# Optimization experiments

Measured on AMD Instinct MI355X. Metric: run time of the kernel, lower is better.

## Reference

```python
import math
import jax, jax.numpy as jnp
import numpy as np

N_EMBD = 768
N_HEAD = 12
BLOCK_SIZE = 1024
B, T, N_ENC = 8, 1024, 257
EPS = 1e-5


def _ln(x, g, b):
    m = jnp.mean(x, axis=-1, keepdims=True)
    v = jnp.var(x, axis=-1, keepdims=True)
    return (x - m) * jax.lax.rsqrt(v + EPS) * g + b


def _heads(t, n_head):
    B_, N_, C_ = t.shape
    return t.reshape(B_, N_, n_head, C_ // n_head).transpose(0, 2, 1, 3)  # [B,H,N,D]


def setup_inputs() -> dict:
    key = jax.random.key(0)
    ks = jax.random.split(key, 16)
    s = 0.02
    d, h4, dq = N_EMBD, 4 * N_EMBD, N_EMBD // 4
    inp = {
        'x': jax.random.normal(ks[0], (B, T, d), jnp.float32),
        'x_enc': jax.random.normal(ks[1], (B, N_ENC, d), jnp.float32),
        'ln1_g': jnp.ones((d,), jnp.float32), 'ln1_b': jnp.zeros((d,), jnp.float32),
        'ln2_g': jnp.ones((d,), jnp.float32), 'ln2_b': jnp.zeros((d,), jnp.float32),
        'ln3_g': jnp.ones((d,), jnp.float32), 'ln3_b': jnp.zeros((d,), jnp.float32),
        'attn_w': jax.random.normal(ks[2], (d, 3 * d), jnp.float32) * s,
        'attn_bias': jnp.zeros((3 * d,), jnp.float32),
        'attn_proj_w': jax.random.normal(ks[3], (d, d), jnp.float32) * s,
        'attn_proj_b': jnp.zeros((d,), jnp.float32),
        'img_w': jax.random.normal(ks[4], (d, 2 * d), jnp.float32) * s,
        'img_b': jnp.zeros((2 * d,), jnp.float32),
        'cap_w': jax.random.normal(ks[5], (d, d), jnp.float32) * s,
        'cap_b': jnp.zeros((d,), jnp.float32),
        'cross_proj_w': jax.random.normal(ks[6], (d, d), jnp.float32) * s,
        'cross_proj_b': jnp.zeros((d,), jnp.float32),
        'ad1_w': jax.random.normal(ks[7], (d, dq), jnp.float32) * s,
        'ad1_b': jnp.zeros((dq,), jnp.float32),
        'ad2_w': jax.random.normal(ks[8], (dq, d), jnp.float32) * s,
        'ad2_b': jnp.zeros((d,), jnp.float32),
        'fc_w': jax.random.normal(ks[9], (d, h4), jnp.float32) * s,
        'fc_b': jnp.zeros((h4,), jnp.float32),
        'mproj_w': jax.random.normal(ks[10], (h4, d), jnp.float32) * s,
        'mproj_b': jnp.zeros((d,), jnp.float32),
    }
    return inp


def _block(x, x_enc, ln1_g, ln1_b, ln2_g, ln2_b, ln3_g, ln3_b,
           attn_w, attn_bias, attn_proj_w, attn_proj_b,
           img_w, img_b, cap_w, cap_b, cross_proj_w, cross_proj_b,
           ad1_w, ad1_b, ad2_w, ad2_b, fc_w, fc_b, mproj_w, mproj_b):
    d, nh = N_EMBD, N_HEAD
    hd = d // nh
    scale = 1.0 / math.sqrt(hd)

    def adapter(h):
        return jax.nn.relu(h @ ad1_w + ad1_b) @ ad2_w + ad2_b

    # --- causal self-attention ---
    h = _ln(x, ln1_g, ln1_b)
    qkv = h @ attn_w + attn_bias
    q, k, v = jnp.split(qkv, 3, axis=2)
    q, k, v = _heads(q, nh), _heads(k, nh), _heads(v, nh)  # [B,H,T,hd]
    att = jnp.einsum('bhqd,bhkd->bhqk', q, k) * scale
    Tq = x.shape[1]
    causal = jnp.tril(jnp.ones((Tq, Tq), bool))
    att = jnp.where(causal, att, -jnp.inf)
    att = jax.nn.softmax(att, axis=-1)
    sa = jnp.einsum('bhqk,bhkd->bhqd', att, v).transpose(0, 2, 1, 3).reshape(x.shape)
    sa = sa @ attn_proj_w + attn_proj_b
    x = x + adapter(sa)

    # --- cross-attention (queries from x, keys/values from x_enc) ---
    hq = _ln(x, ln1_g, ln1_b)
    he = _ln(x_enc, ln3_g, ln3_b)
    kv = he @ img_w + img_b
    k2, v2 = jnp.split(kv, 2, axis=2)
    q2 = hq @ cap_w + cap_b
    q2, k2, v2 = _heads(q2, nh), _heads(k2, nh), _heads(v2, nh)
    catt = jax.nn.softmax(jnp.einsum('bhqd,bhkd->bhqk', q2, k2) * scale, axis=-1)
    ca = jnp.einsum('bhqk,bhkd->bhqd', catt, v2).transpose(0, 2, 1, 3).reshape(x.shape)
    ca = ca @ cross_proj_w + cross_proj_b
    x = x + adapter(ca)

    # --- MLP ---
    hm = _ln(x, ln2_g, ln2_b)
    m = jax.nn.gelu(hm @ fc_w + fc_b, approximate=True) @ mproj_w + mproj_b
    x = x + adapter(m)
    return x, x_enc


def reference(x, x_enc, ln1_g, ln1_b, ln2_g, ln2_b, ln3_g, ln3_b,
              attn_w, attn_bias, attn_proj_w, attn_proj_b,
              img_w, img_b, cap_w, cap_b, cross_proj_w, cross_proj_b,
              ad1_w, ad1_b, ad2_w, ad2_b, fc_w, fc_b, mproj_w, mproj_b):
    return _block(x, x_enc, ln1_g, ln1_b, ln2_g, ln2_b, ln3_g, ln3_b,
                  attn_w, attn_bias, attn_proj_w, attn_proj_b,
                  img_w, img_b, cap_w, cap_b, cross_proj_w, cross_proj_b,
                  ad1_w, ad1_b, ad2_w, ad2_b, fc_w, fc_b, mproj_w, mproj_b)
```

## Files before the change

kernel.cpp:

```cpp
#include <hip/hip_runtime.h>

typedef unsigned short u16;
typedef short bf16x8 __attribute__((ext_vector_type(8)));
typedef float f32x4 __attribute__((ext_vector_type(4)));
typedef unsigned short u16x4 __attribute__((ext_vector_type(4)));

__device__ __forceinline__ u16 f2bf(float f) {
  union { float f; unsigned u; } v; v.f = f;
  unsigned u = v.u;
  unsigned r = (u + 0x7FFFu + ((u >> 16) & 1u)) >> 16;
  return (u16)r;
}
__device__ __forceinline__ float bf2f(u16 h) {
  union { unsigned u; float f; } v; v.u = ((unsigned)h) << 16;
  return v.f;
}
__device__ __forceinline__ unsigned cvt_pk_bf16(float lo, float hi) {
  unsigned d;
  asm("v_cvt_pk_bf16_f32 %0, %1, %2" : "=v"(d) : "v"(lo), "v"(hi));
  return d;
}
__device__ __forceinline__ float gelu_f(float x) {
  const float c1 = -2.302585093f;
  const float c2 = -0.1029620967f;
  float t = __builtin_fmaf(x * x, c2, c1) * x;
  float e = exp2f(t);
  return x * __builtin_amdgcn_rcpf(e + 1.0f);
}

#define GLD_LDS16(gp, lp)                                             \
  __builtin_amdgcn_global_load_lds(                                   \
      (const __attribute__((address_space(1))) void*)(gp),            \
      (__attribute__((address_space(3))) void*)(lp), 16, 0, 0)

template<int OFF>
__device__ __forceinline__ u16x4 tr16(unsigned a) {
  u16x4 d;
  asm volatile("ds_read_b64_tr_b16 %0, %1 offset:%2" : "=&v"(d) : "v"(a), "n"(OFF));
  return d;
}
__device__ __forceinline__ bf16x8 pack8(u16x4 a, u16x4 b) {
  union { u16x4 p[2]; bf16x8 v; } u;
  u.p[0] = a; u.p[1] = b;
  return u.v;
}
__device__ __forceinline__ u16x4 pack4(unsigned w0, unsigned w1) {
  union { unsigned w[2]; u16x4 v; } u;
  u.w[0] = w0; u.w[1] = w1;
  return u.v;
}

struct TrBatch {
  const float* W[9];
  u16* Bt[9];
  int K[9], N[9], Kpad[9], Npad[9];
  int tstart[10];
};
__global__ __launch_bounds__(256)
void transpose_all(TrBatch tb) {
  __shared__ float tile[64][65];
  const int tid = blockIdx.x;
  int mi = 0;
  while (mi < 8 && tid >= tb.tstart[mi + 1]) ++mi;
  const int lt = tid - tb.tstart[mi];
  const int tx = tb.Npad[mi] >> 6;
  const int n0 = (lt % tx) * 64;
  const int k0 = (lt / tx) * 64;
  const float* W = tb.W[mi];
  u16* Bt = tb.Bt[mi];
  const int K = tb.K[mi], N = tb.N[mi], Kpad = tb.Kpad[mi];
  const int t = threadIdx.x;
  const int c = t & 63;
  const int rb = t >> 6;
#pragma unroll
  for (int i = 0; i < 16; ++i) {
    int r = i * 4 + rb;
    float v = 0.f;
    if (k0 + r < K && n0 + c < N) v = W[(size_t)(k0 + r) * N + n0 + c];
    tile[r][c] = v;
  }
  __syncthreads();
#pragma unroll
  for (int i = 0; i < 16; ++i) {
    int r = i * 4 + rb;
    Bt[(size_t)(n0 + r) * Kpad + k0 + c] = f2bf(tile[c][r]);
  }
}

__global__ __launch_bounds__(64)
void ln_kernel(const float* __restrict__ X, const float* __restrict__ G,
               const float* __restrict__ Bv, u16* __restrict__ O, int Mreal) {
  const int row = blockIdx.x;
  const int l = threadIdx.x;
  u16* op = O + (size_t)row * 768;
  if (row >= Mreal) {
    u16x4 z = {0, 0, 0, 0};
#pragma unroll
    for (int i = 0; i < 3; ++i) *(u16x4*)(op + (i * 64 + l) * 4) = z;
    return;
  }
  const float* xp = X + (size_t)row * 768;
  float v[12];
  float s = 0.f, s2 = 0.f;
#pragma unroll
  for (int i = 0; i < 3; ++i) {
    float4 t4 = *(const float4*)(xp + (i * 64 + l) * 4);
    v[i * 4 + 0] = t4.x; v[i * 4 + 1] = t4.y; v[i * 4 + 2] = t4.z; v[i * 4 + 3] = t4.w;
    s += t4.x + t4.y + t4.z + t4.w;
    s2 += t4.x * t4.x + t4.y * t4.y + t4.z * t4.z + t4.w * t4.w;
  }
#pragma unroll
  for (int off = 32; off > 0; off >>= 1) {
    s += __shfl_xor(s, off);
    s2 += __shfl_xor(s2, off);
  }
  const float mean = s * (1.0f / 768.0f);
  const float var = s2 * (1.0f / 768.0f) - mean * mean;
  const float rstd = rsqrtf(var + 1e-5f);
#pragma unroll
  for (int i = 0; i < 3; ++i) {
    int base = (i * 64 + l) * 4;
    float4 g4 = *(const float4*)(G + base);
    float4 b4 = *(const float4*)(Bv + base);
    u16x4 o4;
    o4[0] = f2bf((v[i * 4 + 0] - mean) * rstd * g4.x + b4.x);
    o4[1] = f2bf((v[i * 4 + 1] - mean) * rstd * g4.y + b4.y);
    o4[2] = f2bf((v[i * 4 + 2] - mean) * rstd * g4.z + b4.z);
    o4[3] = f2bf((v[i * 4 + 3] - mean) * rstd * g4.w + b4.w);
    *(u16x4*)(op + base) = o4;
  }
}

template<bool DOLN, bool RESID>
__global__ __launch_bounds__(64)
void resid_ln(const float* __restrict__ S, float* __restrict__ D,
              const u16* __restrict__ P,
              const float* __restrict__ G, const float* __restrict__ Bv,
              u16* __restrict__ O) {
  const int row = blockIdx.x;
  const int l = threadIdx.x;
  const float* sp = S + (size_t)row * 768;
  float* dp = D + (size_t)row * 768;
  float v[12];
  float s = 0.f, s2 = 0.f;
#pragma unroll
  for (int i = 0; i < 3; ++i) {
    const int base = (i * 64 + l) * 4;
    float4 t4 = *(const float4*)(sp + base);
    if (RESID) {
      u16x4 p4 = *(const u16x4*)(P + (size_t)row * 768 + base);
      t4.x += bf2f(p4[0]); t4.y += bf2f(p4[1]);
      t4.z += bf2f(p4[2]); t4.w += bf2f(p4[3]);
    }
    v[i * 4 + 0] = t4.x; v[i * 4 + 1] = t4.y; v[i * 4 + 2] = t4.z; v[i * 4 + 3] = t4.w;
    s += t4.x + t4.y + t4.z + t4.w;
    s2 += t4.x * t4.x + t4.y * t4.y + t4.z * t4.z + t4.w * t4.w;
    *(float4*)(dp + base) = t4;
  }
  if (DOLN) {
#pragma unroll
    for (int off = 32; off > 0; off >>= 1) {
      s += __shfl_xor(s, off);
      s2 += __shfl_xor(s2, off);
    }
    const float mean = s * (1.0f / 768.0f);
    const float var = s2 * (1.0f / 768.0f) - mean * mean;
    const float rstd = rsqrtf(var + 1e-5f);
    u16* op = O + (size_t)row * 768;
#pragma unroll
    for (int i = 0; i < 3; ++i) {
      int base = (i * 64 + l) * 4;
      float4 g4 = *(const float4*)(G + base);
      float4 b4 = *(const float4*)(Bv + base);
      u16x4 o4;
      o4[0] = f2bf((v[i * 4 + 0] - mean) * rstd * g4.x + b4.x);
      o4[1] = f2bf((v[i * 4 + 1] - mean) * rstd * g4.y + b4.y);
      o4[2] = f2bf((v[i * 4 + 2] - mean) * rstd * g4.z + b4.z);
      o4[3] = f2bf((v[i * 4 + 3] - mean) * rstd * g4.w + b4.w);
      *(u16x4*)(op + base) = o4;
    }
  }
}

template<int MODE>
__global__ void gemm_bt(const u16* __restrict__ A, const u16* __restrict__ Bt,
                        void* __restrict__ C, const float* __restrict__ bias,
                        int K, int ldc, int nbias) {
  __shared__ u16 As[2 * 128 * 32];
  __shared__ u16 Bs[2 * 128 * 32];
  const int t = threadIdx.x;
  const int lane = t & 63;
  const int wid = t >> 6;
  const int wm = (wid >> 1) * 64;
  const int wn = (wid & 1) * 64;
  const int tm = blockIdx.x * 128;
  const int tn = blockIdx.y * 128;

  f32x4 zero = {0.f, 0.f, 0.f, 0.f};
  f32x4 acc[4][4];
#pragma unroll
  for (int i = 0; i < 4; ++i)
#pragma unroll
    for (int j = 0; j < 4; ++j) acc[i][j] = zero;

  const int rowA = lane & 15;
  const int kb = (((lane >> 4) ^ ((rowA >> 1) & 3)) << 3);
  const int kTiles = K >> 6;
  for (int kt = 0; kt < kTiles; ++kt) {
    const int kk = kt << 6;
#pragma unroll
    for (int i = 0; i < 4; ++i) {
      const int c = i * 256 + t;
      const int r = (c >> 2) & 127;
      const int cc = ((c >> 9) << 5) + ((((c & 3) ^ ((r >> 1) & 3))) << 3);
      GLD_LDS16(A + (size_t)(tm + r) * K + kk + cc, As + c * 8);
      GLD_LDS16(Bt + (size_t)(tn + r) * K + kk + cc, Bs + c * 8);
    }
    __syncthreads();
#pragma unroll
    for (int ks = 0; ks < 2; ++ks) {
      bf16x8 af[4], bfr[4];
      const int base = ks * 4096;
#pragma unroll
      for (int i = 0; i < 4; ++i) {
        af[i] = *(const bf16x8*)(As + base + (wm + i * 16 + rowA) * 32 + kb);
        bfr[i] = *(const bf16x8*)(Bs + base + (wn + i * 16 + rowA) * 32 + kb);
      }
#pragma unroll
      for (int mi = 0; mi < 4; ++mi)
#pragma unroll
        for (int ni = 0; ni < 4; ++ni)
          acc[mi][ni] = __builtin_amdgcn_mfma_f32_16x16x32_bf16(af[mi], bfr[ni], acc[mi][ni], 0, 0, 0);
    }
    __syncthreads();
  }
  const int col0 = lane & 15;
  const int row0 = (lane >> 4) << 2;
#pragma unroll
  for (int mi = 0; mi < 4; ++mi) {
#pragma unroll
    for (int ni = 0; ni < 4; ++ni) {
      int col = tn + wn + ni * 16 + col0;
      float bb = (col < nbias) ? bias[col] : 0.f;
      float vv[4];
#pragma unroll
      for (int r = 0; r < 4; ++r) {
        float v = acc[mi][ni][r] + bb;
        if (MODE == 1) v = fmaxf(v, 0.f);
        else if (MODE == 2) v = gelu_f(v);
        vv[r] = v;
      }
      unsigned w0 = cvt_pk_bf16(vv[0], vv[1]);
      unsigned w1 = cvt_pk_bf16(vv[2], vv[3]);
      size_t row = (size_t)(tm + wm + mi * 16 + row0);
      u16* cp = (u16*)C + row * ldc + col;
      cp[0] = (u16)w0;
      cp[(size_t)ldc] = (u16)(w0 >> 16);
      cp[(size_t)ldc * 2] = (u16)w1;
      cp[(size_t)ldc * 3] = (u16)(w1 >> 16);
    }
  }
}

template<int MODE>
__global__ __launch_bounds__(256)
void gemm_bt_k128(const u16* __restrict__ A, const u16* __restrict__ Bt,
                  void* __restrict__ C, const float* __restrict__ bias,
                  int K, int ldc, int nbias) {
  __shared__ u16 As[4 * 128 * 32];
  __shared__ u16 Bs[4 * 128 * 32];
  const int t = threadIdx.x;
  const int lane = t & 63;
  const int wid = t >> 6;
  const int wm = (wid >> 1) * 64;
  const int wn = (wid & 1) * 64;
  const int tm = blockIdx.x * 128;
  const int tn = blockIdx.y * 128;

  f32x4 zero = {0.f, 0.f, 0.f, 0.f};
  f32x4 acc[4][4];
#pragma unroll
  for (int i = 0; i < 4; ++i)
#pragma unroll
    for (int j = 0; j < 4; ++j) acc[i][j] = zero;

  const int rowA = lane & 15;
  const int kb = (((lane >> 4) ^ ((rowA >> 1) & 3)) << 3);
  const int kTiles = K >> 7;
  for (int kt = 0; kt < kTiles; ++kt) {
    const int kk = kt << 7;
#pragma unroll
    for (int i = 0; i < 8; ++i) {
      const int c = i * 256 + t;
      const int r = (c >> 2) & 127;
      const int cc = ((c >> 9) << 5) + ((((c & 3) ^ ((r >> 1) & 3))) << 3);
      GLD_LDS16(A + (size_t)(tm + r) * K + kk + cc, As + c * 8);
      GLD_LDS16(Bt + (size_t)(tn + r) * K + kk + cc, Bs + c * 8);
    }
    __syncthreads();
#pragma unroll
    for (int ks = 0; ks < 4; ++ks) {
      bf16x8 af[4], bfr[4];
      const int base = ks * 4096;
#pragma unroll
      for (int i = 0; i < 4; ++i) {
        af[i] = *(const bf16x8*)(As + base + (wm + i * 16 + rowA) * 32 + kb);
        bfr[i] = *(const bf16x8*)(Bs + base + (wn + i * 16 + rowA) * 32 + kb);
      }
#pragma unroll
      for (int mi = 0; mi < 4; ++mi)
#pragma unroll
        for (int ni = 0; ni < 4; ++ni)
          acc[mi][ni] = __builtin_amdgcn_mfma_f32_16x16x32_bf16(af[mi], bfr[ni], acc[mi][ni], 0, 0, 0);
    }
    __syncthreads();
  }
  const int col0 = lane & 15;
  const int row0 = (lane >> 4) << 2;
#pragma unroll
  for (int mi = 0; mi < 4; ++mi) {
#pragma unroll
    for (int ni = 0; ni < 4; ++ni) {
      int col = tn + wn + ni * 16 + col0;
      float bb = (col < nbias) ? bias[col] : 0.f;
      float vv[4];
#pragma unroll
      for (int r = 0; r < 4; ++r) {
        float v = acc[mi][ni][r] + bb;
        if (MODE == 1) v = fmaxf(v, 0.f);
        vv[r] = v;
      }
      unsigned w0 = cvt_pk_bf16(vv[0], vv[1]);
      unsigned w1 = cvt_pk_bf16(vv[2], vv[3]);
      size_t row = (size_t)(tm + wm + mi * 16 + row0);
      u16* cp = (u16*)C + row * ldc + col;
      cp[0] = (u16)w0;
      cp[(size_t)ldc] = (u16)(w0 >> 16);
      cp[(size_t)ldc * 2] = (u16)w1;
      cp[(size_t)ldc * 3] = (u16)(w1 >> 16);
    }
  }
}

struct GemmJob {
  const u16* A; const u16* Bt; u16* C; const float* bias;
  int K, ldc, nbias, mblocks;
};
__global__ __launch_bounds__(256)
void gemm_bt_dual(GemmJob j0, GemmJob j1, int split) {
  __shared__ u16 As[2 * 128 * 32];
  __shared__ u16 Bs[2 * 128 * 32];
  const int bid = blockIdx.x;
  const GemmJob& J = (bid < split) ? j0 : j1;
  const int lb = (bid < split) ? bid : bid - split;
  const int tm = (lb % J.mblocks) * 128;
  const int tn = (lb / J.mblocks) * 128;
  const u16* A = J.A;
  const u16* Bt = J.Bt;
  const int K = J.K;

  const int t = threadIdx.x;
  const int lane = t & 63;
  const int wid = t >> 6;
  const int wm = (wid >> 1) * 64;
  const int wn = (wid & 1) * 64;

  f32x4 zero = {0.f, 0.f, 0.f, 0.f};
  f32x4 acc[4][4];
#pragma unroll
  for (int i = 0; i < 4; ++i)
#pragma unroll
    for (int j = 0; j < 4; ++j) acc[i][j] = zero;

  const int rowA = lane & 15;
  const int kb = (((lane >> 4) ^ ((rowA >> 1) & 3)) << 3);
  const int kTiles = K >> 6;
  for (int kt = 0; kt < kTiles; ++kt) {
    const int kk = kt << 6;
#pragma unroll
    for (int i = 0; i < 4; ++i) {
      const int c = i * 256 + t;
      const int r = (c >> 2) & 127;
      const int cc = ((c >> 9) << 5) + ((((c & 3) ^ ((r >> 1) & 3))) << 3);
      GLD_LDS16(A + (size_t)(tm + r) * K + kk + cc, As + c * 8);
      GLD_LDS16(Bt + (size_t)(tn + r) * K + kk + cc, Bs + c * 8);
    }
    __syncthreads();
#pragma unroll
    for (int ks = 0; ks < 2; ++ks) {
      bf16x8 af[4], bfr[4];
      const int base = ks * 4096;
#pragma unroll
      for (int i = 0; i < 4; ++i) {
        af[i] = *(const bf16x8*)(As + base + (wm + i * 16 + rowA) * 32 + kb);
        bfr[i] = *(const bf16x8*)(Bs + base + (wn + i * 16 + rowA) * 32 + kb);
      }
#pragma unroll
      for (int mi = 0; mi < 4; ++mi)
#pragma unroll
        for (int ni = 0; ni < 4; ++ni)
          acc[mi][ni] = __builtin_amdgcn_mfma_f32_16x16x32_bf16(af[mi], bfr[ni], acc[mi][ni], 0, 0, 0);
    }
    __syncthreads();
  }
  const int col0 = lane & 15;
  const int row0 = (lane >> 4) << 2;
#pragma unroll
  for (int mi = 0; mi < 4; ++mi) {
#pragma unroll
    for (int ni = 0; ni < 4; ++ni) {
      int col = tn + wn + ni * 16 + col0;
      float bb = (col < J.nbias) ? J.bias[col] : 0.f;
      unsigned w0 = cvt_pk_bf16(acc[mi][ni][0] + bb, acc[mi][ni][1] + bb);
      unsigned w1 = cvt_pk_bf16(acc[mi][ni][2] + bb, acc[mi][ni][3] + bb);
      size_t row = (size_t)(tm + wm + mi * 16 + row0);
      u16* cp = J.C + row * J.ldc + col;
      cp[0] = (u16)w0;
      cp[(size_t)J.ldc] = (u16)(w0 >> 16);
      cp[(size_t)J.ldc * 2] = (u16)w1;
      cp[(size_t)J.ldc * 3] = (u16)(w1 >> 16);
    }
  }
}

template<bool CAUSAL>
__global__ __launch_bounds__(256)
void attn_mfma(const u16* __restrict__ Q, const u16* __restrict__ Kp,
               const u16* __restrict__ Vp,
               u16* __restrict__ O0, u16* __restrict__ O1, float2* __restrict__ ML,
               int seqkv, int qrs, int krs,
               long long qBatch, long long kBatch,
               int qoff, int koff, int voff) {
  __shared__ __align__(16) u16 Ks[64 * 64];
  __shared__ __align__(16) u16 Vs[4096];
  __shared__ __align__(16) u16 Ps[4][1024];
  const int t = threadIdx.x;
  const int lane = t & 63;
  const int wid = t >> 6;
  const int b = blockIdx.x / 12, h = blockIdx.x % 12;
  const int yq = CAUSAL ? ((int)gridDim.y - 1 - (int)blockIdx.y) : (int)blockIdx.y;
  const int q0 = yq * 64;
  const int colid = lane & 15;
  const int rgrp = lane >> 4;
  const int z = CAUSAL ? blockIdx.z : 0;

  int kt_begin = 0, kt_end;
  if (CAUSAL) {
    const int ntr = yq + 1;
    const int half = (ntr + 1) >> 1;
    kt_begin = z ? half : 0;
    kt_end = z ? ntr : half;
  } else {
    kt_end = (seqkv + 63) >> 6;
  }
  u16* Op = (CAUSAL && z) ? O1 : O0;

  if (CAUSAL && kt_begin >= kt_end) {
    if (colid == 0) {
#pragma unroll
      for (int r = 0; r < 4; ++r) {
        int qrow = q0 + wid * 16 + rgrp * 4 + r;
        ML[((size_t)z * 8192 + b * 1024 + qrow) * 12 + h] = make_float2(-1e30f, 0.f);
      }
    }
    return;
  }

  const u16* qp = Q + (size_t)b * qBatch + qoff + (size_t)(q0 + wid * 16 + colid) * qrs + h * 64;
  bf16x8 qa[2];
#pragma unroll
  for (int s = 0; s < 2; ++s) qa[s] = *(const bf16x8*)(qp + s * 32 + (rgrp << 3));

  f32x4 oacc[4];
#pragma unroll
  for (int i = 0; i < 4; ++i) oacc[i] = (f32x4){0.f, 0.f, 0.f, 0.f};
  float m[4] = {-1e30f, -1e30f, -1e30f, -1e30f};
  float l[4] = {0.f, 0.f, 0.f, 0.f};

  const u16* kbase = Kp + (size_t)b * kBatch + koff + h * 64;
  const u16* vbase = Vp + (size_t)b * kBatch + voff + h * 64;

  const int srr = t >> 3, sdc = t & 7;
  int kwo[2], vwo[2];
#pragma unroll
  for (int i = 0; i < 2; ++i) {
    const int r = srr + 32 * i;
    kwo[i] = r * 64 + ((sdc ^ (r & 7)) << 3);
    vwo[i] = ((sdc >> 1) << 10) + (i << 9) + (((srr >> 2) & 1) << 8)
           + (((srr >> 3) & 3) << 6) + ((srr & 3) << 4) + (((2 * sdc) & 3) << 2);
  }
  const unsigned vs_base = (unsigned)(size_t)&Vs[0] + 8u * (unsigned)lane;
  const unsigned ps_base = (unsigned)(size_t)&Ps[wid][0] + 8u * (unsigned)lane;

  bf16x8 kz[2], vz[2];
  auto LOADT = [&](int kt) {
    const int k0 = kt * 64;
#pragma unroll
    for (int i = 0; i < 2; ++i) {
      const int tk = k0 + srr + 32 * i;
      const int dc = sdc << 3;
      kz[i] = (bf16x8){0, 0, 0, 0, 0, 0, 0, 0};
      vz[i] = (bf16x8){0, 0, 0, 0, 0, 0, 0, 0};
      if (tk < seqkv) {
        kz[i] = *(const bf16x8*)(kbase + (size_t)tk * krs + dc);
        vz[i] = *(const bf16x8*)(vbase + (size_t)tk * krs + dc);
      }
    }
  };
  LOADT(kt_begin);

  constexpr float SC2 = 0.18033688011112042f;

  for (int kt = kt_begin; kt < kt_end; ++kt) {
    const int k0 = kt * 64;
#pragma unroll
    for (int i = 0; i < 2; ++i) {
      *(bf16x8*)&Ks[kwo[i]] = kz[i];
      *(bf16x8*)&Vs[vwo[i]] = vz[i];
    }
    __syncthreads();
    if (kt + 1 < kt_end) LOADT(kt + 1);

    f32x4 sacc[4];
#pragma unroll
    for (int c = 0; c < 4; ++c) sacc[c] = (f32x4){0.f, 0.f, 0.f, 0.f};
#pragma unroll
    for (int c = 0; c < 4; ++c)
#pragma unroll
      for (int s = 0; s < 2; ++s) {
        bf16x8 kf = *(const bf16x8*)&Ks[(c * 16 + colid) * 64 +
                                        ((((s << 2) + rgrp) ^ (colid & 7)) << 3)];
        sacc[c] = __builtin_amdgcn_mfma_f32_16x16x32_bf16(qa[s], kf, sacc[c], 0, 0, 0);
      }

    const bool domask = CAUSAL ? (kt == yq) : (kt == kt_end - 1);
    if (domask) {
#pragma unroll
      for (int c = 0; c < 4; ++c) {
        int kv = k0 + c * 16 + colid;
#pragma unroll
        for (int r = 0; r < 4; ++r) {
          int q = q0 + wid * 16 + rgrp * 4 + r;
          if ((CAUSAL && kv > q) || (!CAUSAL && kv >= seqkv)) sacc[c][r] = -1e30f;
        }
      }
    }

    float pms[4];
#pragma unroll
    for (int r = 0; r < 4; ++r) {
      float v = fmaxf(fmaxf(sacc[0][r], sacc[1][r]), fmaxf(sacc[2][r], sacc[3][r]));
#pragma unroll
      for (int off = 1; off < 16; off <<= 1) v = fmaxf(v, __shfl_xor(v, off));
      pms[r] = v * SC2;
    }
    bool ok = (pms[0] <= m[0] + 8.f) && (pms[1] <= m[1] + 8.f) &&
              (pms[2] <= m[2] + 8.f) && (pms[3] <= m[3] + 8.f);
    if (!__all(ok)) {
#pragma unroll
      for (int r = 0; r < 4; ++r) {
        float newm = fmaxf(m[r], pms[r]);
        float corr = exp2f(m[r] - newm);
        m[r] = newm;
        l[r] *= corr;
#pragma unroll
        for (int dc2 = 0; dc2 < 4; ++dc2) oacc[dc2][r] *= corr;
      }
    }

    float pv[4][4];
    float psum[4] = {0.f, 0.f, 0.f, 0.f};
#pragma unroll
    for (int c = 0; c < 4; ++c)
#pragma unroll
      for (int r = 0; r < 4; ++r) {
        float p = exp2f(__builtin_fmaf(sacc[c][r], SC2, -m[r]));
        pv[c][r] = p;
        psum[r] += p;
      }
#pragma unroll
    for (int r = 0; r < 4; ++r) {
#pragma unroll
      for (int off = 1; off < 16; off <<= 1) psum[r] += __shfl_xor(psum[r], off);
      l[r] += psum[r];
    }

#pragma unroll
    for (int c = 0; c < 4; ++c) {
      unsigned w0 = cvt_pk_bf16(pv[c][0], pv[c][1]);
      unsigned w1 = cvt_pk_bf16(pv[c][2], pv[c][3]);
      const int pa = ((c >> 1) << 9) + (((colid >> 2) & 1) << 8)
                   + (((2 * c + (colid >> 3)) & 3) << 6) + ((colid & 3) << 4) + (rgrp << 2);
      *(u16x4*)&Ps[wid][pa] = pack4(w0, w1);
    }
    __builtin_amdgcn_sched_barrier(0);

    u16x4 p00 = tr16<0>(ps_base);
    u16x4 p01 = tr16<512>(ps_base);
    u16x4 p10 = tr16<1024>(ps_base);
    u16x4 p11 = tr16<1536>(ps_base);
    asm volatile("s_waitcnt lgkmcnt(0)" ::: "memory");
    __builtin_amdgcn_sched_barrier(0);
    bf16x8 pf0 = pack8(p00, p01);
    bf16x8 pf1 = pack8(p10, p11);

#pragma unroll
    for (int dc2 = 0; dc2 < 4; ++dc2) {
      const unsigned va = vs_base + (unsigned)(dc2 * 2048);
      u16x4 v00 = tr16<0>(va);
      u16x4 v01 = tr16<512>(va);
      u16x4 v10 = tr16<1024>(va);
      u16x4 v11 = tr16<1536>(va);
      asm volatile("s_waitcnt lgkmcnt(0)" ::: "memory");
      __builtin_amdgcn_sched_barrier(0);
      bf16x8 vf0 = pack8(v00, v01);
      bf16x8 vf1 = pack8(v10, v11);
      oacc[dc2] = __builtin_amdgcn_mfma_f32_16x16x32_bf16(pf0, vf0, oacc[dc2], 0, 0, 0);
      oacc[dc2] = __builtin_amdgcn_mfma_f32_16x16x32_bf16(pf1, vf1, oacc[dc2], 0, 0, 0);
    }
    __syncthreads();
  }

#pragma unroll
  for (int r = 0; r < 4; ++r) {
    int qrow = q0 + wid * 16 + rgrp * 4 + r;
    u16* op = Op + ((size_t)b * 1024 + qrow) * 768 + h * 64;
    if (CAUSAL) {
      unsigned w0 = cvt_pk_bf16(oacc[0][r], oacc[1][r]);
      unsigned w1 = cvt_pk_bf16(oacc[2][r], oacc[3][r]);
      op[colid] = (u16)w0;
      op[16 + colid] = (u16)(w0 >> 16);
      op[32 + colid] = (u16)w1;
      op[48 + colid] = (u16)(w1 >> 16);
      if (colid == 0)
        ML[((size_t)z * 8192 + b * 1024 + qrow) * 12 + h] = make_float2(m[r], l[r]);
    } else {
      float inv = 1.f / l[r];
      unsigned w0 = cvt_pk_bf16(oacc[0][r] * inv, oacc[1][r] * inv);
      unsigned w1 = cvt_pk_bf16(oacc[2][r] * inv, oacc[3][r] * inv);
      op[colid] = (u16)w0;
      op[16 + colid] = (u16)(w0 >> 16);
      op[32 + colid] = (u16)w1;
      op[48 + colid] = (u16)(w1 >> 16);
    }
  }
}

__global__ __launch_bounds__(64)
void attn_combine(const u16* __restrict__ P0, const u16* __restrict__ P1,
                  const float2* __restrict__ ML, u16* __restrict__ O) {
  const int row = blockIdx.x;
  const int l = threadIdx.x;
#pragma unroll
  for (int i = 0; i < 3; ++i) {
    const int base = (i * 64 + l) * 4;
    const int h = base >> 6;
    float2 ml0 = ML[(size_t)row * 12 + h];
    float2 ml1 = ML[(size_t)8192 * 12 + row * 12 + h];
    float mm = fmaxf(ml0.x, ml1.x);
    float w0 = exp2f(ml0.x - mm);
    float w1 = exp2f(ml1.x - mm);
    float inv = 1.f / (ml0.y * w0 + ml1.y * w1);
    u16x4 a = *(const u16x4*)(P0 + (size_t)row * 768 + base);
    u16x4 c = *(const u16x4*)(P1 + (size_t)row * 768 + base);
    u16x4 o4;
#pragma unroll
    for (int j = 0; j < 4; ++j)
      o4[j] = f2bf((bf2f(a[j]) * w0 + bf2f(c[j]) * w1) * inv);
    *(u16x4*)(O + (size_t)row * 768 + base) = o4;
  }
}

extern "C" void kernel_launch(void* const* d_in, const int* in_sizes, int n_in,
                              void* d_out, int out_size, void* d_ws, size_t ws_size,
                              hipStream_t stream) {
  const float* x        = (const float*)d_in[0];
  const float* x_enc    = (const float*)d_in[1];
  const float* ln1_g    = (const float*)d_in[2];
  const float* ln1_b    = (const float*)d_in[3];
  const float* ln2_g    = (const float*)d_in[4];
  const float* ln2_b    = (const float*)d_in[5];
  const float* ln3_g    = (const float*)d_in[6];
  const float* ln3_b    = (const float*)d_in[7];
  const float* attn_w   = (const float*)d_in[8];
  const float* attn_bias= (const float*)d_in[9];
  const float* proj_w   = (const float*)d_in[10];
  const float* proj_b   = (const float*)d_in[11];
  const float* img_w    = (const float*)d_in[12];
  const float* img_b    = (const float*)d_in[13];
  const float* cap_w    = (const float*)d_in[14];
  const float* cap_b    = (const float*)d_in[15];
  const float* cross_w  = (const float*)d_in[16];
  const float* cross_b  = (const float*)d_in[17];
  const float* ad1_w    = (const float*)d_in[18];
  const float* ad1_b    = (const float*)d_in[19];
  const float* ad2_w    = (const float*)d_in[20];
  const float* ad2_b    = (const float*)d_in[21];
  const float* fc_w     = (const float*)d_in[22];
  const float* fc_b     = (const float*)d_in[23];
  const float* mproj_w  = (const float*)d_in[24];
  const float* mproj_b  = (const float*)d_in[25];

  const int Mx = 8192;
  const int Me = 2056;
  const int MeP = 2176;

  float* out_x  = (float*)d_out;
  float* out_xe = out_x + (size_t)Mx * 768;

  char* ws = (char*)d_ws;
  size_t off = 0;
  auto alloc = [&](size_t elems) {
    u16* p = (u16*)(ws + off);
    off = (off + elems * 2 + 255) & ~(size_t)255;
    return p;
  };
  u16* wt_attn  = alloc((size_t)2304 * 768);
  u16* wt_proj  = alloc((size_t)768 * 768);
  u16* wt_img   = alloc((size_t)1536 * 768);
  u16* wt_cap   = alloc((size_t)768 * 768);
  u16* wt_cross = alloc((size_t)768 * 768);
  u16* wt_ad1   = alloc((size_t)256 * 768);
  u16* wt_ad2   = alloc((size_t)768 * 256);
  u16* wt_fc    = alloc((size_t)3072 * 768);
  u16* wt_mproj = alloc((size_t)768 * 3072);
  u16* hbuf     = alloc((size_t)Mx * 768);
  u16* big      = alloc((size_t)Mx * 3072);
  u16* p0       = alloc((size_t)Mx * 768);
  u16* p1       = alloc((size_t)Mx * 768);
  u16* hid      = alloc((size_t)Mx * 256);
  float2* mlbuf = (float2*)alloc((size_t)2 * 8192 * 12 * 4);
  u16* q2  = big;
  u16* kvb = big + (size_t)Mx * 768;

  hipMemcpyAsync(out_xe, x_enc, (size_t)Me * 768 * 4, hipMemcpyDeviceToDevice, stream);

  TrBatch tb;
  int nt = 0;
  tb.tstart[0] = 0;
  auto addT = [&](const float* W, u16* Bt, int K, int N, int Kp, int Np) {
    tb.W[nt] = W; tb.Bt[nt] = Bt; tb.K[nt] = K; tb.N[nt] = N;
    tb.Kpad[nt] = Kp; tb.Npad[nt] = Np;
    tb.tstart[nt + 1] = tb.tstart[nt] + (Np / 64) * (Kp / 64);
    ++nt;
  };
  addT(attn_w, wt_attn, 768, 2304, 768, 2304);
  addT(proj_w, wt_proj, 768, 768, 768, 768);
  addT(img_w, wt_img, 768, 1536, 768, 1536);
  addT(cap_w, wt_cap, 768, 768, 768, 768);
  addT(cross_w, wt_cross, 768, 768, 768, 768);
  addT(ad1_w, wt_ad1, 768, 192, 768, 256);
  addT(ad2_w, wt_ad2, 192, 768, 256, 768);
  addT(fc_w, wt_fc, 768, 3072, 768, 3072);
  addT(mproj_w, wt_mproj, 3072, 768, 3072, 768);
  transpose_all<<<tb.tstart[9], 256, 0, stream>>>(tb);

  auto GEMM = [&](const u16* A, const u16* Bt, void* C, const float* bias,
                  int M, int N, int K, int ldc, int nbias, int mode) {
    dim3 g(M / 128, N / 128);
    if (mode == 0)      gemm_bt<0><<<g, 256, 0, stream>>>(A, Bt, C, bias, K, ldc, nbias);
    else if (mode == 1) gemm_bt<1><<<g, 256, 0, stream>>>(A, Bt, C, bias, K, ldc, nbias);
    else                gemm_bt<2><<<g, 256, 0, stream>>>(A, Bt, C, bias, K, ldc, nbias);
  };
  auto GEMM_K128 = [&](const u16* A, const u16* Bt, void* C, const float* bias,
                       int M, int N, int K, int ldc, int nbias, int mode) {
    dim3 g(M / 128, N / 128);
    if (mode == 0) gemm_bt_k128<0><<<g, 256, 0, stream>>>(A, Bt, C, bias, K, ldc, nbias);
    else           gemm_bt_k128<1><<<g, 256, 0, stream>>>(A, Bt, C, bias, K, ldc, nbias);
  };
  auto ADAPTER = [&](const u16* in, u16* padw) {
    GEMM_K128(in, wt_ad1, hid, ad1_b, Mx, 256, 768, 256, 192, 1);
    GEMM_K128(hid, wt_ad2, padw, ad2_b, Mx, 768, 256, 768, 768, 0);
  };

  resid_ln<true, false><<<Mx, 64, 0, stream>>>(x, out_x, nullptr, ln1_g, ln1_b, hbuf);

  GEMM(hbuf, wt_attn, big, attn_bias, Mx, 2304, 768, 2304, 2304, 0);
  attn_mfma<true><<<dim3(96, 16, 2), 256, 0, stream>>>(
      big, big, big, hbuf, p1, mlbuf, 1024, 2304, 2304,
      (long long)1024 * 2304, (long long)1024 * 2304, 0, 768, 1536);
  attn_combine<<<Mx, 64, 0, stream>>>(hbuf, p1, mlbuf, p0);
  GEMM_K128(p0, wt_proj, p1, proj_b, Mx, 768, 768, 768, 768, 0);
  ADAPTER(p1, p0);
  resid_ln<true, true><<<Mx, 64, 0, stream>>>(out_x, out_x, p0, ln1_g, ln1_b, hbuf);

  ln_kernel<<<MeP, 64, 0, stream>>>(x_enc, ln3_g, ln3_b, p0, Me);
  {
    GemmJob jkv = { p0,   wt_img, kvb, img_b, 768, 1536, 1536, MeP / 128 };
    GemmJob jq2 = { hbuf, wt_cap, q2,  cap_b, 768, 768,  768,  Mx / 128 };
    const int split = (MeP / 128) * (1536 / 128);
    const int total = split + (Mx / 128) * (768 / 128);
    gemm_bt_dual<<<total, 256, 0, stream>>>(jkv, jq2, split);
  }
  attn_mfma<false><<<dim3(96, 16), 256, 0, stream>>>(
      q2, kvb, kvb, p1, nullptr, nullptr, 257, 768, 1536,
      (long long)1024 * 768, (long long)257 * 1536, 0, 0, 768);
  GEMM_K128(p1, wt_cross, p0, cross_b, Mx, 768, 768, 768, 768, 0);
  ADAPTER(p0, p1);
  resid_ln<true, true><<<Mx, 64, 0, stream>>>(out_x, out_x, p1, ln2_g, ln2_b, hbuf);

  GEMM(hbuf, wt_fc, big, fc_b, Mx, 3072, 768, 3072, 3072, 2);
  GEMM_K128(big, wt_mproj, p0, mproj_b, Mx, 768, 3072, 768, 768, 0);
  ADAPTER(p0, p1);
  resid_ln<false, true><<<Mx, 64, 0, stream>>>(out_x, out_x, p1, nullptr, nullptr, nullptr);

  (void)in_sizes; (void)n_in; (void)out_size; (void)ws_size;
}
```

Measured before the change: 468.9 us.

## Double-buffer LDS in K128 GEMM with async prefetch of next K tile

Replaces the single-buffered 128-wide K tile GEMM with a double-buffered 64-wide K tile kernel. It issues global-to-LDS loads for the next tile before computing the current one, and uses vmcnt waits and raw barriers instead of syncthreads. The goal is to overlap memory latency with MFMA work in the projection, adapter and mproj GEMMs. LDS use stays the same, but each buffer has half the K depth, so the kernel runs more loop iterations and more barriers.

```diff
diff --git a/kernel.cpp b/kernel.cpp
--- a/kernel.cpp
+++ b/kernel.cpp
@@ -264,11 +264,11 @@
 
 template<int MODE>
 __global__ __launch_bounds__(256)
-void gemm_bt_k128(const u16* __restrict__ A, const u16* __restrict__ Bt,
-                  void* __restrict__ C, const float* __restrict__ bias,
-                  int K, int ldc, int nbias) {
-  __shared__ u16 As[4 * 128 * 32];
-  __shared__ u16 Bs[4 * 128 * 32];
+void gemm_bt_pf(const u16* __restrict__ A, const u16* __restrict__ Bt,
+                void* __restrict__ C, const float* __restrict__ bias,
+                int K, int ldc, int nbias) {
+  __shared__ u16 As[2][2 * 128 * 32];
+  __shared__ u16 Bs[2][2 * 128 * 32];
   const int t = threadIdx.x;
   const int lane = t & 63;
   const int wid = t >> 6;
@@ -284,28 +284,48 @@
 #pragma unroll
     for (int j = 0; j < 4; ++j) acc[i][j] = zero;
 
+  const u16* agp[4]; const u16* bgp[4]; int lofs[4];
+#pragma unroll
+  for (int i = 0; i < 4; ++i) {
+    const int c = i * 256 + t;
+    const int r = (c >> 2) & 127;
+    const int cc = ((c >> 9) << 5) + ((((c & 3) ^ ((r >> 1) & 3))) << 3);
+    agp[i] = A + (size_t)(tm + r) * K + cc;
+    bgp[i] = Bt + (size_t)(tn + r) * K + cc;
+    lofs[i] = c * 8;
+  }
+  auto STAGE = [&](int buf, int kt) {
+    const int kk = kt << 6;
+#pragma unroll
+    for (int i = 0; i < 4; ++i) {
+      GLD_LDS16(agp[i] + kk, &As[buf][lofs[i]]);
+      GLD_LDS16(bgp[i] + kk, &Bs[buf][lofs[i]]);
+    }
+  };
+
   const int rowA = lane & 15;
   const int kb = (((lane >> 4) ^ ((rowA >> 1) & 3)) << 3);
-  const int kTiles = K >> 7;
+  const int kTiles = K >> 6;
+
+  STAGE(0, 0);
+  int cur = 0;
   for (int kt = 0; kt < kTiles; ++kt) {
-    const int kk = kt << 7;
-#pragma unroll
-    for (int i = 0; i < 8; ++i) {
-      const int c = i * 256 + t;
-      const int r = (c >> 2) & 127;
-      const int cc = ((c >> 9) << 5) + ((((c & 3) ^ ((r >> 1) & 3))) << 3);
-      GLD_LDS16(A + (size_t)(tm + r) * K + kk + cc, As + c * 8);
-      GLD_LDS16(Bt + (size_t)(tn + r) * K + kk + cc, Bs + c * 8);
-    }
-    __syncthreads();
-#pragma unroll
-    for (int ks = 0; ks < 4; ++ks) {
+    if (kt + 1 < kTiles) {
+      STAGE(cur ^ 1, kt + 1);
+      asm volatile("s_waitcnt vmcnt(8)" ::: "memory");
+    } else {
+      asm volatile("s_waitcnt vmcnt(0)" ::: "memory");
+    }
+    __builtin_amdgcn_s_barrier();
+    __builtin_amdgcn_sched_barrier(0);
+#pragma unroll
+    for (int ks = 0; ks < 2; ++ks) {
       bf16x8 af[4], bfr[4];
       const int base = ks * 4096;
 #pragma unroll
       for (int i = 0; i < 4; ++i) {
-        af[i] = *(const bf16x8*)(As + base + (wm + i * 16 + rowA) * 32 + kb);
-        bfr[i] = *(const bf16x8*)(Bs + base + (wn + i * 16 + rowA) * 32 + kb);
+        af[i] = *(const bf16x8*)(&As[cur][base + (wm + i * 16 + rowA) * 32 + kb]);
+        bfr[i] = *(const bf16x8*)(&Bs[cur][base + (wn + i * 16 + rowA) * 32 + kb]);
       }
 #pragma unroll
       for (int mi = 0; mi < 4; ++mi)
@@ -313,8 +333,11 @@
         for (int ni = 0; ni < 4; ++ni)
           acc[mi][ni] = __builtin_amdgcn_mfma_f32_16x16x32_bf16(af[mi], bfr[ni], acc[mi][ni], 0, 0, 0);
     }
-    __syncthreads();
-  }
+    __builtin_amdgcn_sched_barrier(0);
+    __builtin_amdgcn_s_barrier();
+    cur ^= 1;
+  }
+
   const int col0 = lane & 15;
   const int row0 = (lane >> 4) << 2;
 #pragma unroll
@@ -328,6 +351,7 @@
       for (int r = 0; r < 4; ++r) {
         float v = acc[mi][ni][r] + bb;
         if (MODE == 1) v = fmaxf(v, 0.f);
+        else if (MODE == 2) v = gelu_f(v);
         vv[r] = v;
       }
       unsigned w0 = cvt_pk_bf16(vv[0], vv[1]);
@@ -762,15 +786,15 @@
     else if (mode == 1) gemm_bt<1><<<g, 256, 0, stream>>>(A, Bt, C, bias, K, ldc, nbias);
     else                gemm_bt<2><<<g, 256, 0, stream>>>(A, Bt, C, bias, K, ldc, nbias);
   };
-  auto GEMM_K128 = [&](const u16* A, const u16* Bt, void* C, const float* bias,
-                       int M, int N, int K, int ldc, int nbias, int mode) {
+  auto GEMM_PF = [&](const u16* A, const u16* Bt, void* C, const float* bias,
+                     int M, int N, int K, int ldc, int nbias, int mode) {
     dim3 g(M / 128, N / 128);
-    if (mode == 0) gemm_bt_k128<0><<<g, 256, 0, stream>>>(A, Bt, C, bias, K, ldc, nbias);
-    else           gemm_bt_k128<1><<<g, 256, 0, stream>>>(A, Bt, C, bias, K, ldc, nbias);
+    if (mode == 0) gemm_bt_pf<0><<<g, 256, 0, stream>>>(A, Bt, C, bias, K, ldc, nbias);
+    else           gemm_bt_pf<1><<<g, 256, 0, stream>>>(A, Bt, C, bias, K, ldc, nbias);
   };
   auto ADAPTER = [&](const u16* in, u16* padw) {
-    GEMM_K128(in, wt_ad1, hid, ad1_b, Mx, 256, 768, 256, 192, 1);
-    GEMM_K128(hid, wt_ad2, padw, ad2_b, Mx, 768, 256, 768, 768, 0);
+    GEMM_PF(in, wt_ad1, hid, ad1_b, Mx, 256, 768, 256, 192, 1);
+    GEMM_PF(hid, wt_ad2, padw, ad2_b, Mx, 768, 256, 768, 768, 0);
   };
 
   resid_ln<true, false><<<Mx, 64, 0, stream>>>(x, out_x, nullptr, ln1_g, ln1_b, hbuf);
@@ -780,7 +804,7 @@
       big, big, big, hbuf, p1, mlbuf, 1024, 2304, 2304,
       (long long)1024 * 2304, (long long)1024 * 2304, 0, 768, 1536);
   attn_combine<<<Mx, 64, 0, stream>>>(hbuf, p1, mlbuf, p0);
-  GEMM_K128(p0, wt_proj, p1, proj_b, Mx, 768, 768, 768, 768, 0);
+  GEMM_PF(p0, wt_proj, p1, proj_b, Mx, 768, 768, 768, 768, 0);
   ADAPTER(p1, p0);
   resid_ln<true, true><<<Mx, 64, 0, stream>>>(out_x, out_x, p0, ln1_g, ln1_b, hbuf);
 
@@ -795,12 +819,12 @@
   attn_mfma<false><<<dim3(96, 16), 256, 0, stream>>>(
       q2, kvb, kvb, p1, nullptr, nullptr, 257, 768, 1536,
       (long long)1024 * 768, (long long)257 * 1536, 0, 0, 768);
-  GEMM_K128(p1, wt_cross, p0, cross_b, Mx, 768, 768, 768, 768, 0);
+  GEMM_PF(p1, wt_cross, p0, cross_b, Mx, 768, 768, 768, 768, 0);
   ADAPTER(p0, p1);
   resid_ln<true, true><<<Mx, 64, 0, stream>>>(out_x, out_x, p1, ln2_g, ln2_b, hbuf);
 
   GEMM(hbuf, wt_fc, big, fc_b, Mx, 3072, 768, 3072, 3072, 2);
-  GEMM_K128(big, wt_mproj, p0, mproj_b, Mx, 768, 3072, 768, 768, 0);
+  GEMM_PF(big, wt_mproj, p0, mproj_b, Mx, 768, 3072, 768, 768, 0);
   ADAPTER(p0, p1);
   resid_ln<false, true><<<Mx, 64, 0, stream>>>(out_x, out_x, p1, nullptr, nullptr, nullptr);
 
```

Measured after the change: 471.6 us. Within noise of the previous version (+0.6%).
